# Performance work log

Measured on AMD Instinct MI355X. Metric: run time of the kernel, lower is better.

Reference implementation:

```python
import jax, jax.numpy as jnp
import numpy as np
from jax import lax

B = 16
DEPTH = 24
D_MODEL = 192
D_INNER = 384   # expand=2
D_STATE = 16
D_CONV = 4
DT_RANK = 12    # ceil(192/16)
PATCH = 16
EPS = 1e-5


def setup_inputs() -> dict:
    key = jax.random.key(0)
    ks = jax.random.split(key, 24)
    def n(k, shape, s):
        return jax.random.normal(k, shape, jnp.float32) * s
    inp = {}
    inp["x_img"] = jax.random.normal(ks[0], (B, 3, 256, 256), jnp.float32)
    inp["z_img"] = jax.random.normal(ks[1], (B, 3, 128, 128), jnp.float32)
    # patch embed conv
    inp["patch_w"] = n(ks[2], (D_MODEL, 3, PATCH, PATCH), 0.02)
    inp["patch_b"] = jnp.zeros((D_MODEL,), jnp.float32)
    # abs pos embeds (token counts fixed by module: 256 for x, 64 for z)
    inp["pos_x"] = n(ks[3], (1, 256, D_MODEL), 0.02)
    inp["pos_z"] = n(ks[4], (1, 64, D_MODEL), 0.02)
    # per-layer norms (LayerNorm, rms_norm=False)
    inp["ln_w"] = jnp.ones((DEPTH, D_MODEL), jnp.float32)
    inp["ln_b"] = jnp.zeros((DEPTH, D_MODEL), jnp.float32)
    # Mamba mixer params (stacked over depth)
    inp["in_w"] = n(ks[5], (DEPTH, 2 * D_INNER, D_MODEL), 0.05)          # in_proj (no bias)
    inp["conv_w"] = n(ks[6], (DEPTH, D_INNER, D_CONV), 0.2)              # depthwise conv1d
    inp["conv_b"] = jnp.zeros((DEPTH, D_INNER), jnp.float32)
    inp["xproj_w"] = n(ks[7], (DEPTH, DT_RANK + 2 * D_STATE, D_INNER), 0.05)  # x_proj (no bias)
    inp["dt_w"] = n(ks[8], (DEPTH, D_INNER, DT_RANK), 0.1)               # dt_proj weight
    # dt bias ~ inverse-softplus of dt in [1e-3, 0.1] (Mamba init)
    dt = jnp.exp(jax.random.uniform(ks[9], (DEPTH, D_INNER)) * (np.log(0.1) - np.log(1e-3)) + np.log(1e-3))
    inp["dt_b"] = dt + jnp.log(-jnp.expm1(-dt))
    # A_log init: log(1..d_state) per channel
    inp["A_log"] = jnp.log(jnp.tile(jnp.arange(1, D_STATE + 1, dtype=jnp.float32), (DEPTH, D_INNER, 1)))
    inp["D_skip"] = jnp.ones((DEPTH, D_INNER), jnp.float32)
    inp["out_w"] = n(ks[10], (DEPTH, D_MODEL, D_INNER), 0.05)            # out_proj (no bias)
    inp["fnorm_w"] = jnp.ones((D_MODEL,), jnp.float32)
    inp["fnorm_b"] = jnp.zeros((D_MODEL,), jnp.float32)
    return inp


def _layer_norm(x, w, b):
    mu = jnp.mean(x, axis=-1, keepdims=True)
    var = jnp.mean(jnp.square(x - mu), axis=-1, keepdims=True)
    return (x - mu) * lax.rsqrt(var + EPS) * w + b


def _patch_embed(img, w, b):
    # Conv2d stride=patch, then flatten HW -> tokens
    y = lax.conv_general_dilated(img, w, (PATCH, PATCH), 'VALID',
                                 dimension_numbers=('NCHW', 'OIHW', 'NCHW'))
    y = y + b[None, :, None, None]
    Bn, D, H, W = y.shape
    return y.reshape(Bn, D, H * W).transpose(0, 2, 1)  # (B, HW, D)


def _ssm_scan(dA, dBu):
    # h_t = dA_t * h_{t-1} + dBu_t, parallel over time via associative scan
    def comb(e1, e2):
        a1, b1 = e1
        a2, b2 = e2
        return a2 * a1, a2 * b1 + b2
    _, h = lax.associative_scan(comb, (dA, dBu), axis=1)
    return h  # (B, L, D_INNER, D_STATE)


def _mamba(h, in_w, conv_w, conv_b, xproj_w, dt_w, dt_b, A_log, D_skip, out_w):
    # h: (B, L, D_MODEL)
    xz = h @ in_w.T                                   # (B, L, 2*D_INNER)
    xc, zg = jnp.split(xz, 2, axis=-1)
    # causal depthwise conv over time
    xt = xc.transpose(0, 2, 1)                        # (B, D_INNER, L)
    xt = lax.conv_general_dilated(xt, conv_w[:, None, :], (1,), [(D_CONV - 1, 0)],
                                  feature_group_count=D_INNER,
                                  dimension_numbers=('NCH', 'OIH', 'NCH'))
    xt = xt + conv_b[None, :, None]
    xc = jax.nn.silu(xt).transpose(0, 2, 1)           # (B, L, D_INNER)
    dbl = xc @ xproj_w.T                              # (B, L, dt_rank + 2*d_state)
    dt, Bm, Cm = jnp.split(dbl, [DT_RANK, DT_RANK + D_STATE], axis=-1)
    dt = jax.nn.softplus(dt @ dt_w.T + dt_b)          # (B, L, D_INNER)
    A = -jnp.exp(A_log)                               # (D_INNER, D_STATE)
    dA = jnp.exp(dt[..., None] * A)                   # (B, L, D_INNER, D_STATE)
    dBu = dt[..., None] * Bm[:, :, None, :] * xc[..., None]
    hs = _ssm_scan(dA, dBu)
    y = jnp.einsum('bldn,bln->bld', hs, Cm) + xc * D_skip
    y = y * jax.nn.silu(zg)
    return y @ out_w.T                                # (B, L, D_MODEL)


def reference(x_img, z_img, patch_w, patch_b, pos_x, pos_z, ln_w, ln_b,
              in_w, conv_w, conv_b, xproj_w, dt_w, dt_b, A_log, D_skip,
              out_w, fnorm_w, fnorm_b):
    x_tok = _patch_embed(x_img, patch_w, patch_b) + pos_x   # (B, 256, D)
    z_tok = _patch_embed(z_img, patch_w, patch_b) + pos_z   # (B, 64, D)
    hidden = jnp.concatenate([z_tok, x_tok], axis=1)        # (B, 320, D)
    residual = None
    for i in range(DEPTH):
        # fused add-norm prenorm: residual = hidden + residual; hidden = LN(residual)
        residual = hidden if residual is None else hidden + residual
        h_n = _layer_norm(residual, ln_w[i], ln_b[i])
        hidden = _mamba(h_n, in_w[i], conv_w[i], conv_b[i], xproj_w[i],
                        dt_w[i], dt_b[i], A_log[i], D_skip[i], out_w[i])
    residual = residual + hidden
    return _layer_norm(residual, fnorm_w, fnorm_b)          # (B, 320, D), final_pool_type='none'
```

## Files before the change

### kernel.cpp

```cpp
#include <hip/hip_runtime.h>
#include <hip/hip_bf16.h>

#define BB 16
#define DEPTH 24
#define DM 192
#define DI 384
#define DS 16
#define DC 4
#define DTR 12
#define LL 320
#define NX 256
#define NZ 64
#define NT (BB * LL)
#define NC 10
#define LC 32
#define EPSV 1e-5f

__device__ inline float siluf(float x) { return x / (1.f + __expf(-x)); }
__device__ inline float softplusf(float x) {
    return (x > 20.f) ? x : log1pf(expf(x));
}
__device__ inline float wave_sum64(float v) {
    #pragma unroll
    for (int o = 32; o > 0; o >>= 1) v += __shfl_xor(v, o);
    return v;
}

__global__ __launch_bounds__(256) void ln_gemm(const float* __restrict__ hidden,
                                               const float* __restrict__ resin,
                                               float* __restrict__ resout,
                                               const float* __restrict__ lnw,
                                               const float* __restrict__ lnb,
                                               size_t lnoff,
                                               const float* __restrict__ w,
                                               size_t woff,
                                               float* __restrict__ out,
                                               int first) {
    __shared__ float xs[32][196];
    __shared__ float ws[128][52];
    int t0 = blockIdx.x * 32;
    int j0 = blockIdx.y * 128;
    {
        int tt = threadIdx.x >> 3;
        int l8 = threadIdx.x & 7;
        size_t base = (size_t)(t0 + tt) * DM;
        float v[24];
        float s = 0.f;
        #pragma unroll
        for (int j = 0; j < 24; j++) {
            int e = l8 + 8 * j;
            float x = hidden[base + e];
            if (!first) x += resin[base + e];
            v[j] = x;
            s += x;
        }
        s += __shfl_xor(s, 1); s += __shfl_xor(s, 2); s += __shfl_xor(s, 4);
        float mu = s * (1.f / 192.f);
        float q = 0.f;
        #pragma unroll
        for (int j = 0; j < 24; j++) { float d = v[j] - mu; q += d * d; }
        q += __shfl_xor(q, 1); q += __shfl_xor(q, 2); q += __shfl_xor(q, 4);
        float inv = rsqrtf(q * (1.f / 192.f) + EPSV);
        #pragma unroll
        for (int j = 0; j < 24; j++) {
            int e = l8 + 8 * j;
            if (blockIdx.y == 0) resout[base + e] = v[j];
            xs[tt][e] = (v[j] - mu) * inv * lnw[lnoff + e] + lnb[lnoff + e];
        }
    }
    __syncthreads();
    int lane = threadIdx.x & 63;
    int wv = threadIdx.x >> 6;
    float acc[8][2];
    #pragma unroll
    for (int t = 0; t < 8; t++) { acc[t][0] = 0.f; acc[t][1] = 0.f; }
    for (int kt = 0; kt < 192; kt += 48) {
        for (int idx = threadIdx.x; idx < 128 * 12; idx += 256) {
            int jj = idx / 12, kc = idx % 12;
            float4 v4 = *(const float4*)&w[woff + (size_t)(j0 + jj) * 192 + kt + kc * 4];
            *(float4*)&ws[jj][kc * 4] = v4;
        }
        __syncthreads();
        #pragma unroll 2
        for (int kk = 0; kk < 48; kk += 4) {
            float4 xv[8];
            #pragma unroll
            for (int t = 0; t < 8; t++)
                xv[t] = *(const float4*)&xs[wv * 8 + t][kt + kk];
            #pragma unroll
            for (int o = 0; o < 2; o++) {
                float4 wv4 = *(const float4*)&ws[lane + 64 * o][kk];
                #pragma unroll
                for (int t = 0; t < 8; t++)
                    acc[t][o] += xv[t].x * wv4.x + xv[t].y * wv4.y
                               + xv[t].z * wv4.z + xv[t].w * wv4.w;
            }
        }
        __syncthreads();
    }
    #pragma unroll
    for (int t = 0; t < 8; t++)
        #pragma unroll
        for (int o = 0; o < 2; o++)
            out[(size_t)(t0 + wv * 8 + t) * 768 + j0 + lane + 64 * o] = acc[t][o];
}

template<int K, int KT, int NO>
__global__ __launch_bounds__(256) void gemm_rt(const float* __restrict__ x,
                                               const float* __restrict__ w,
                                               size_t woff,
                                               float* __restrict__ out, int N) {
    constexpr int NCOL = 64 * NO;
    constexpr int KC = KT / 4;
    __shared__ float xs[32][KT + 4];
    __shared__ float ws[NCOL][KT + 4];
    int t0 = blockIdx.x * 32;
    int j0 = blockIdx.y * NCOL;
    int lane = threadIdx.x & 63;
    int wv = threadIdx.x >> 6;
    float acc[8][NO];
    #pragma unroll
    for (int t = 0; t < 8; t++)
        #pragma unroll
        for (int o = 0; o < NO; o++) acc[t][o] = 0.f;

    for (int kt = 0; kt < K; kt += KT) {
        for (int idx = threadIdx.x; idx < 32 * KC; idx += 256) {
            int tt = idx / KC, kc = idx % KC;
            float4 v = *(const float4*)&x[(size_t)(t0 + tt) * K + kt + kc * 4];
            *(float4*)&xs[tt][kc * 4] = v;
        }
        for (int idx = threadIdx.x; idx < NCOL * KC; idx += 256) {
            int jj = idx / KC, kc = idx % KC;
            float4 v = *(const float4*)&w[woff + (size_t)(j0 + jj) * K + kt + kc * 4];
            *(float4*)&ws[jj][kc * 4] = v;
        }
        __syncthreads();
        #pragma unroll 2
        for (int kk = 0; kk < KT; kk += 4) {
            float4 xv[8];
            #pragma unroll
            for (int t = 0; t < 8; t++)
                xv[t] = *(const float4*)&xs[wv * 8 + t][kk];
            #pragma unroll
            for (int o = 0; o < NO; o++) {
                float4 wv4 = *(const float4*)&ws[lane + 64 * o][kk];
                #pragma unroll
                for (int t = 0; t < 8; t++)
                    acc[t][o] += xv[t].x * wv4.x + xv[t].y * wv4.y
                               + xv[t].z * wv4.z + xv[t].w * wv4.w;
            }
        }
        __syncthreads();
    }
    #pragma unroll
    for (int t = 0; t < 8; t++)
        #pragma unroll
        for (int o = 0; o < NO; o++)
            out[(size_t)(t0 + wv * 8 + t) * N + j0 + lane + 64 * o] = acc[t][o];
}

__global__ __launch_bounds__(256) void patch_rt(const float* __restrict__ x_img,
                                                const float* __restrict__ z_img,
                                                const float* __restrict__ w,
                                                const float* __restrict__ bias,
                                                const float* __restrict__ pos_x,
                                                const float* __restrict__ pos_z,
                                                float* __restrict__ hidden) {
    __shared__ float xs[32][100];
    __shared__ float ws[64][100];
    bool isx = blockIdx.x < (BB * NX / 32);
    const float* img = isx ? x_img : z_img;
    const float* pos = isx ? pos_x : pos_z;
    int side = isx ? 16 : 8;
    int tok_off = isx ? NZ : 0;
    int ntok = side * side;
    int pt0 = (isx ? blockIdx.x : blockIdx.x - BB * NX / 32) * 32;
    int j0 = blockIdx.y * 64;
    int S = side * 16;
    int lane = threadIdx.x & 63;
    int wv = threadIdx.x >> 6;
    float acc[8];
    #pragma unroll
    for (int t = 0; t < 8; t++) acc[t] = 0.f;

    for (int kt = 0; kt < 768; kt += 96) {
        for (int idx = threadIdx.x; idx < 32 * 24; idx += 256) {
            int tt = idx / 24, kc = idx % 24;
            int k = kt + kc * 4;
            int c = k >> 8, p = k & 255, pi = p >> 4, pj = p & 15;
            int patch = pt0 + tt;
            int b = patch / ntok, t = patch % ntok;
            int ph = t / side, pw = t % side;
            float4 v = *(const float4*)&img[((size_t)(b * 3 + c) * S + ph * 16 + pi) * S
                                            + pw * 16 + pj];
            *(float4*)&xs[tt][kc * 4] = v;
        }
        for (int idx = threadIdx.x; idx < 64 * 24; idx += 256) {
            int jj = idx / 24, kc = idx % 24;
            float4 v = *(const float4*)&w[(size_t)(j0 + jj) * 768 + kt + kc * 4];
            *(float4*)&ws[jj][kc * 4] = v;
        }
        __syncthreads();
        #pragma unroll 2
        for (int kk = 0; kk < 96; kk += 4) {
            float4 xv[8];
            #pragma unroll
            for (int t = 0; t < 8; t++)
                xv[t] = *(const float4*)&xs[wv * 8 + t][kk];
            float4 wv4 = *(const float4*)&ws[lane][kk];
            #pragma unroll
            for (int t = 0; t < 8; t++)
                acc[t] += xv[t].x * wv4.x + xv[t].y * wv4.y
                        + xv[t].z * wv4.z + xv[t].w * wv4.w;
        }
        __syncthreads();
    }
    float bj = bias[j0 + lane];
    #pragma unroll
    for (int t = 0; t < 8; t++) {
        int patch = pt0 + wv * 8 + t;
        int b = patch / ntok, tk = patch % ntok;
        hidden[((size_t)b * LL + tok_off + tk) * DM + j0 + lane] =
            acc[t] + bj + pos[(size_t)tk * DM + j0 + lane];
    }
}

__global__ __launch_bounds__(256) void xpd_kernel(const float* __restrict__ xz,
                                                  const float* __restrict__ cw,
                                                  const float* __restrict__ cb,
                                                  const float* __restrict__ xpw,
                                                  const float* __restrict__ dtw,
                                                  const float* __restrict__ dtbias,
                                                  float* __restrict__ xc,
                                                  float* __restrict__ dbl,
                                                  float* __restrict__ dtbuf,
                                                  int layer) {
    __shared__ float smem[5760];
    float* xs   = smem;
    float* ws   = smem + 832;
    float* sdbl = smem;
    float* sdtw = smem + 768;

    int t0 = blockIdx.x * 16;
    int l0 = t0 % LL;
    int lane = threadIdx.x & 63;
    int wv = threadIdx.x >> 6;
    const float* cwl = cw  + (size_t)layer * DI * DC;
    const float* cbl = cb  + (size_t)layer * DI;
    const float* xpl = xpw + (size_t)layer * 44 * DI;
    float acc[4] = {0.f, 0.f, 0.f, 0.f};

    for (int kt = 0; kt < DI; kt += 48) {
        for (int idx = threadIdx.x; idx < 16 * 48; idx += 256) {
            int tt = idx / 48, kk = idx % 48;
            int d = kt + kk;
            float a = cbl[d];
            #pragma unroll
            for (int r = 0; r < 4; r++) {
                int l = l0 + tt - 3 + r;
                float v = (l >= 0) ? xz[(size_t)(t0 + tt - 3 + r) * 768 + d] : 0.f;
                a += cwl[d * 4 + r] * v;
            }
            a = siluf(a);
            xs[tt * 52 + kk] = a;
            xc[(size_t)(t0 + tt) * DI + d] = a;
        }
        for (int idx = threadIdx.x; idx < 64 * 12; idx += 256) {
            int jj = idx / 12, kc = idx % 12;
            float4 v = make_float4(0.f, 0.f, 0.f, 0.f);
            if (jj < 44)
                v = *(const float4*)&xpl[(size_t)jj * DI + kt + kc * 4];
            *(float4*)&ws[jj * 52 + kc * 4] = v;
        }
        __syncthreads();
        const float* wr0 = ws + lane * 52;
        #pragma unroll 4
        for (int kk = 0; kk < 48; kk += 4) {
            float4 xv0 = *(const float4*)&xs[(wv * 4 + 0) * 52 + kk];
            float4 xv1 = *(const float4*)&xs[(wv * 4 + 1) * 52 + kk];
            float4 xv2 = *(const float4*)&xs[(wv * 4 + 2) * 52 + kk];
            float4 xv3 = *(const float4*)&xs[(wv * 4 + 3) * 52 + kk];
            float4 wv4 = *(const float4*)&wr0[kk];
            acc[0] += xv0.x * wv4.x + xv0.y * wv4.y + xv0.z * wv4.z + xv0.w * wv4.w;
            acc[1] += xv1.x * wv4.x + xv1.y * wv4.y + xv1.z * wv4.z + xv1.w * wv4.w;
            acc[2] += xv2.x * wv4.x + xv2.y * wv4.y + xv2.z * wv4.z + xv2.w * wv4.w;
            acc[3] += xv3.x * wv4.x + xv3.y * wv4.y + xv3.z * wv4.z + xv3.w * wv4.w;
        }
        __syncthreads();
    }
    if (lane < 44) {
        #pragma unroll
        for (int t = 0; t < 4; t++) {
            sdbl[(wv * 4 + t) * 48 + lane] = acc[t];
            dbl[(size_t)(t0 + wv * 4 + t) * 44 + lane] = acc[t];
        }
    }
    const float* dwl = dtw + (size_t)layer * DI * DTR;
    for (int idx = threadIdx.x; idx < DI * DTR; idx += 256) {
        int d = idx / 12, r = idx % 12;
        sdtw[d * 13 + r] = dwl[idx];
    }
    __syncthreads();
    const float* dbb = dtbias + (size_t)layer * DI;
    for (int idx = threadIdx.x; idx < 16 * DI; idx += 256) {
        int tt = idx / DI, d = idx % DI;
        float a = dbb[d];
        const float* br = sdbl + tt * 48;
        const float* wr = sdtw + d * 13;
        #pragma unroll
        for (int r = 0; r < 12; r++) a += br[r] * wr[r];
        dtbuf[(size_t)(t0 + tt) * DI + d] = softplusf(a);
    }
}

__global__ __launch_bounds__(256) void scanA(const float* __restrict__ dt,
                                             const float* __restrict__ xc,
                                             const float* __restrict__ dbl,
                                             const float* __restrict__ A_log,
                                             float* __restrict__ Pout,
                                             float* __restrict__ Hout,
                                             size_t aoff) {
    int Q = blockIdx.x * 64 + (threadIdx.x >> 2);
    int n0 = threadIdx.x & 3;
    int d = Q % DI;
    int bc = Q / DI;
    int b = bc / NC, c = bc % NC;
    float4 Al = *(const float4*)&A_log[aoff + (size_t)d * DS + n0 * 4];
    float A0 = -expf(Al.x), A1 = -expf(Al.y), A2 = -expf(Al.z), A3 = -expf(Al.w);
    float h0 = 0.f, h1 = 0.f, h2 = 0.f, h3 = 0.f;
    float P0 = 1.f, P1 = 1.f, P2 = 1.f, P3 = 1.f;
    int tbase = b * LL + c * LC;
    for (int l = 0; l < LC; l++) {
        size_t t = (size_t)tbase + l;
        float dtv = dt[t * DI + d];
        float xcv = xc[t * DI + d];
        float4 B4 = *(const float4*)&dbl[t * 44 + DTR + n0 * 4];
        float s = dtv * xcv;
        float e0 = __expf(dtv * A0), e1 = __expf(dtv * A1);
        float e2 = __expf(dtv * A2), e3 = __expf(dtv * A3);
        h0 = e0 * h0 + s * B4.x;  P0 *= e0;
        h1 = e1 * h1 + s * B4.y;  P1 *= e1;
        h2 = e2 * h2 + s * B4.z;  P2 *= e2;
        h3 = e3 * h3 + s * B4.w;  P3 *= e3;
    }
    size_t gi = (size_t)Q * 16 + n0 * 4;
    *(float4*)&Pout[gi] = make_float4(P0, P1, P2, P3);
    *(float4*)&Hout[gi] = make_float4(h0, h1, h2, h3);
}

__global__ __launch_bounds__(256) void scanC(const float* __restrict__ dt,
                                             const float* xc,
                                             const float* __restrict__ dbl,
                                             const float* __restrict__ xz,
                                             const float* __restrict__ A_log,
                                             const float* __restrict__ Dskip,
                                             const float* __restrict__ Pin,
                                             const float* __restrict__ Hin,
                                             float* y,
                                             size_t aoff, size_t doff) {
    int Q = blockIdx.x * 64 + (threadIdx.x >> 2);
    int n0 = threadIdx.x & 3;
    int d = Q % DI;
    int bc = Q / DI;
    int b = bc / NC, c = bc % NC;
    float h0 = 0.f, h1 = 0.f, h2 = 0.f, h3 = 0.f;
    for (int cc = 0; cc < c; cc++) {
        size_t gi = ((size_t)(b * NC + cc) * DI + d) * 16 + n0 * 4;
        float4 P4 = *(const float4*)&Pin[gi];
        float4 H4 = *(const float4*)&Hin[gi];
        h0 = P4.x * h0 + H4.x;
        h1 = P4.y * h1 + H4.y;
        h2 = P4.z * h2 + H4.z;
        h3 = P4.w * h3 + H4.w;
    }
    float4 Al = *(const float4*)&A_log[aoff + (size_t)d * DS + n0 * 4];
    float A0 = -expf(Al.x), A1 = -expf(Al.y), A2 = -expf(Al.z), A3 = -expf(Al.w);
    float Dv = Dskip[doff + d];
    int tbase = b * LL + c * LC;
    for (int l = 0; l < LC; l++) {
        size_t t = (size_t)tbase + l;
        float dtv = dt[t * DI + d];
        float xcv = xc[t * DI + d];
        float4 B4 = *(const float4*)&dbl[t * 44 + DTR + n0 * 4];
        float4 C4 = *(const float4*)&dbl[t * 44 + DTR + DS + n0 * 4];
        float s = dtv * xcv;
        float e0 = __expf(dtv * A0), e1 = __expf(dtv * A1);
        float e2 = __expf(dtv * A2), e3 = __expf(dtv * A3);
        h0 = e0 * h0 + s * B4.x;
        h1 = e1 * h1 + s * B4.y;
        h2 = e2 * h2 + s * B4.z;
        h3 = e3 * h3 + s * B4.w;
        float p = h0 * C4.x + h1 * C4.y + h2 * C4.z + h3 * C4.w;
        p += __shfl_xor(p, 1);
        p += __shfl_xor(p, 2);
        if (n0 == 0) {
            float zg = xz[t * (2 * DI) + DI + d];
            y[t * DI + d] = (p + xcv * Dv) * siluf(zg);
        }
    }
}

__global__ __launch_bounds__(256) void final_kernel(const float* __restrict__ hidden,
                                                    const float* __restrict__ residual,
                                                    const float* __restrict__ w,
                                                    const float* __restrict__ bias,
                                                    float* __restrict__ out) {
    int t = blockIdx.x * 4 + (threadIdx.x >> 6);
    int lane = threadIdx.x & 63;
    size_t base = (size_t)t * DM;
    float a = residual[base + lane]       + hidden[base + lane];
    float b = residual[base + 64 + lane]  + hidden[base + 64 + lane];
    float c = residual[base + 128 + lane] + hidden[base + 128 + lane];
    float mu = wave_sum64(a + b + c) * (1.f / 192.f);
    float va = a - mu, vb = b - mu, vc = c - mu;
    float var = wave_sum64(va * va + vb * vb + vc * vc) * (1.f / 192.f);
    float inv = rsqrtf(var + EPSV);
    out[base + lane]       = va * inv * w[lane]       + bias[lane];
    out[base + 64 + lane]  = vb * inv * w[64 + lane]  + bias[64 + lane];
    out[base + 128 + lane] = vc * inv * w[128 + lane] + bias[128 + lane];
}

extern "C" void kernel_launch(void* const* d_in, const int* in_sizes, int n_in,
                              void* d_out, int out_size, void* d_ws, size_t ws_size,
                              hipStream_t stream) {
    const float* x_img   = (const float*)d_in[0];
    const float* z_img   = (const float*)d_in[1];
    const float* patch_w = (const float*)d_in[2];
    const float* patch_b = (const float*)d_in[3];
    const float* pos_x   = (const float*)d_in[4];
    const float* pos_z   = (const float*)d_in[5];
    const float* ln_w    = (const float*)d_in[6];
    const float* ln_b    = (const float*)d_in[7];
    const float* in_w    = (const float*)d_in[8];
    const float* conv_w  = (const float*)d_in[9];
    const float* conv_b  = (const float*)d_in[10];
    const float* xproj_w = (const float*)d_in[11];
    const float* dt_w    = (const float*)d_in[12];
    const float* dt_b    = (const float*)d_in[13];
    const float* A_log   = (const float*)d_in[14];
    const float* D_skip  = (const float*)d_in[15];
    const float* out_w   = (const float*)d_in[16];
    const float* fnorm_w = (const float*)d_in[17];
    const float* fnorm_b = (const float*)d_in[18];

    float* hidden   = (float*)d_ws;
    float* residual = hidden   + (size_t)NT * DM;
    float* xz       = residual + (size_t)NT * DM;
    float* xc       = xz       + (size_t)NT * 2 * DI;
    float* dbl      = xc       + (size_t)NT * DI;
    float* dtbuf    = dbl      + (size_t)NT * 44;
    float* scanP    = dtbuf    + (size_t)NT * DI;
    float* scanH    = scanP    + (size_t)BB * NC * DI * 16;
    float* yb       = xc;
    float* resalt   = (float*)d_out;

    {
        dim3 gp((BB * NX + BB * NZ) / 32, 3);
        patch_rt<<<gp, 256, 0, stream>>>(x_img, z_img, patch_w, patch_b,
                                         pos_x, pos_z, hidden);
    }

    const int scan_blocks = BB * NC * DI / 64;
    for (int i = 0; i < DEPTH; i++) {
        const float* resin = (i % 2) ? resalt : residual;
        float* resout      = (i % 2) ? residual : resalt;
        {
            dim3 g(NT / 32, 6);
            ln_gemm<<<g, 256, 0, stream>>>(
                hidden, resin, resout, ln_w, ln_b, (size_t)i * DM,
                in_w, (size_t)i * 768 * 192, xz, i == 0 ? 1 : 0);
        }
        xpd_kernel<<<NT / 16, 256, 0, stream>>>(
            xz, conv_w, conv_b, xproj_w, dt_w, dt_b, xc, dbl, dtbuf, i);
        scanA<<<scan_blocks, 256, 0, stream>>>(
            dtbuf, xc, dbl, A_log, scanP, scanH, (size_t)i * DI * DS);
        scanC<<<scan_blocks, 256, 0, stream>>>(
            dtbuf, xc, dbl, xz, A_log, D_skip, scanP, scanH, yb,
            (size_t)i * DI * DS, (size_t)i * DI);
        {
            dim3 g(NT / 32, 3);
            gemm_rt<384, 96, 1><<<g, 256, 0, stream>>>(
                yb, out_w, (size_t)i * 192 * 384, hidden, 192);
        }
    }

    final_kernel<<<NT / 4, 256, 0, stream>>>(hidden, residual, fnorm_w, fnorm_b,
                                             (float*)d_out);
}
```

Measured before the change: 4.285 ms.

## Use 4x4 register micro-tiles in GEMM kernels and halve out-proj/patch block size

Reworks the thread-to-output mapping in the LN+in_proj GEMM, the out_proj GEMM and the patch-embed GEMM so each thread computes a 4x4 tile (4 tokens by 4 columns) instead of 8 tokens by one or two columns. This balances shared-memory loads between x and w fragments and increases FMA per LDS. The out_proj and patch kernels now run with 128 threads per block (2 waves) covering the same 32x64 tile. The trade-off is fewer waves per block to hide latency, and strided global stores (8 lanes per row) instead of fully contiguous 64-wide rows.

```diff
diff --git a/kernel.cpp b/kernel.cpp
--- a/kernel.cpp
+++ b/kernel.cpp
@@ -71,9 +71,13 @@
     __syncthreads();
     int lane = threadIdx.x & 63;
     int wv = threadIdx.x >> 6;
-    float acc[8][2];
-    #pragma unroll
-    for (int t = 0; t < 8; t++) { acc[t][0] = 0.f; acc[t][1] = 0.f; }
+    int r = lane >> 3;
+    int c = lane & 7;
+    float acc[4][4];
+    #pragma unroll
+    for (int i = 0; i < 4; i++)
+        #pragma unroll
+        for (int j = 0; j < 4; j++) acc[i][j] = 0.f;
     for (int kt = 0; kt < 192; kt += 48) {
         for (int idx = threadIdx.x; idx < 128 * 12; idx += 256) {
             int jj = idx / 12, kc = idx % 12;
@@ -83,90 +87,91 @@
         __syncthreads();
         #pragma unroll 2
         for (int kk = 0; kk < 48; kk += 4) {
-            float4 xv[8];
-            #pragma unroll
-            for (int t = 0; t < 8; t++)
-                xv[t] = *(const float4*)&xs[wv * 8 + t][kt + kk];
-            #pragma unroll
-            for (int o = 0; o < 2; o++) {
-                float4 wv4 = *(const float4*)&ws[lane + 64 * o][kk];
+            float4 xv[4];
+            #pragma unroll
+            for (int i = 0; i < 4; i++)
+                xv[i] = *(const float4*)&xs[r + 8 * i][kt + kk];
+            #pragma unroll
+            for (int j = 0; j < 4; j++) {
+                float4 w4 = *(const float4*)&ws[wv * 32 + c + 8 * j][kk];
                 #pragma unroll
-                for (int t = 0; t < 8; t++)
-                    acc[t][o] += xv[t].x * wv4.x + xv[t].y * wv4.y
-                               + xv[t].z * wv4.z + xv[t].w * wv4.w;
+                for (int i = 0; i < 4; i++)
+                    acc[i][j] += xv[i].x * w4.x + xv[i].y * w4.y
+                               + xv[i].z * w4.z + xv[i].w * w4.w;
             }
         }
         __syncthreads();
     }
     #pragma unroll
-    for (int t = 0; t < 8; t++)
-        #pragma unroll
-        for (int o = 0; o < 2; o++)
-            out[(size_t)(t0 + wv * 8 + t) * 768 + j0 + lane + 64 * o] = acc[t][o];
-}
-
-template<int K, int KT, int NO>
-__global__ __launch_bounds__(256) void gemm_rt(const float* __restrict__ x,
-                                               const float* __restrict__ w,
-                                               size_t woff,
-                                               float* __restrict__ out, int N) {
-    constexpr int NCOL = 64 * NO;
+    for (int i = 0; i < 4; i++)
+        #pragma unroll
+        for (int j = 0; j < 4; j++)
+            out[(size_t)(t0 + r + 8 * i) * 768 + j0 + wv * 32 + c + 8 * j] = acc[i][j];
+}
+
+template<int K, int KT>
+__global__ __launch_bounds__(128) void gemm_rt2(const float* __restrict__ x,
+                                                const float* __restrict__ w,
+                                                size_t woff,
+                                                float* __restrict__ out, int N) {
     constexpr int KC = KT / 4;
     __shared__ float xs[32][KT + 4];
-    __shared__ float ws[NCOL][KT + 4];
+    __shared__ float ws[64][KT + 4];
     int t0 = blockIdx.x * 32;
-    int j0 = blockIdx.y * NCOL;
+    int j0 = blockIdx.y * 64;
     int lane = threadIdx.x & 63;
     int wv = threadIdx.x >> 6;
-    float acc[8][NO];
-    #pragma unroll
-    for (int t = 0; t < 8; t++)
-        #pragma unroll
-        for (int o = 0; o < NO; o++) acc[t][o] = 0.f;
+    int r = lane >> 3;
+    int c = lane & 7;
+    float acc[4][4];
+    #pragma unroll
+    for (int i = 0; i < 4; i++)
+        #pragma unroll
+        for (int j = 0; j < 4; j++) acc[i][j] = 0.f;
 
     for (int kt = 0; kt < K; kt += KT) {
-        for (int idx = threadIdx.x; idx < 32 * KC; idx += 256) {
+        for (int idx = threadIdx.x; idx < 32 * KC; idx += 128) {
             int tt = idx / KC, kc = idx % KC;
-            float4 v = *(const float4*)&x[(size_t)(t0 + tt) * K + kt + kc * 4];
-            *(float4*)&xs[tt][kc * 4] = v;
-        }
-        for (int idx = threadIdx.x; idx < NCOL * KC; idx += 256) {
+            *(float4*)&xs[tt][kc * 4] =
+                *(const float4*)&x[(size_t)(t0 + tt) * K + kt + kc * 4];
+        }
+        for (int idx = threadIdx.x; idx < 64 * KC; idx += 128) {
             int jj = idx / KC, kc = idx % KC;
-            float4 v = *(const float4*)&w[woff + (size_t)(j0 + jj) * K + kt + kc * 4];
-            *(float4*)&ws[jj][kc * 4] = v;
+            *(float4*)&ws[jj][kc * 4] =
+                *(const float4*)&w[woff + (size_t)(j0 + jj) * K + kt + kc * 4];
         }
         __syncthreads();
         #pragma unroll 2
         for (int kk = 0; kk < KT; kk += 4) {
-            float4 xv[8];
-            #pragma unroll
-            for (int t = 0; t < 8; t++)
-                xv[t] = *(const float4*)&xs[wv * 8 + t][kk];
-            #pragma unroll
-            for (int o = 0; o < NO; o++) {
-                float4 wv4 = *(const float4*)&ws[lane + 64 * o][kk];
+            float4 xv[4];
+            #pragma unroll
+            for (int i = 0; i < 4; i++)
+                xv[i] = *(const float4*)&xs[r + 8 * i][kk];
+            #pragma unroll
+            for (int j = 0; j < 4; j++) {
+                float4 w4 = *(const float4*)&ws[wv * 32 + c + 8 * j][kk];
                 #pragma unroll
-                for (int t = 0; t < 8; t++)
-                    acc[t][o] += xv[t].x * wv4.x + xv[t].y * wv4.y
-                               + xv[t].z * wv4.z + xv[t].w * wv4.w;
+                for (int i = 0; i < 4; i++)
+                    acc[i][j] += xv[i].x * w4.x + xv[i].y * w4.y
+                               + xv[i].z * w4.z + xv[i].w * w4.w;
             }
         }
         __syncthreads();
     }
     #pragma unroll
-    for (int t = 0; t < 8; t++)
-        #pragma unroll
-        for (int o = 0; o < NO; o++)
-            out[(size_t)(t0 + wv * 8 + t) * N + j0 + lane + 64 * o] = acc[t][o];
-}
-
-__global__ __launch_bounds__(256) void patch_rt(const float* __restrict__ x_img,
-                                                const float* __restrict__ z_img,
-                                                const float* __restrict__ w,
-                                                const float* __restrict__ bias,
-                                                const float* __restrict__ pos_x,
-                                                const float* __restrict__ pos_z,
-                                                float* __restrict__ hidden) {
+    for (int i = 0; i < 4; i++)
+        #pragma unroll
+        for (int j = 0; j < 4; j++)
+            out[(size_t)(t0 + r + 8 * i) * N + j0 + wv * 32 + c + 8 * j] = acc[i][j];
+}
+
+__global__ __launch_bounds__(128) void patch_rt2(const float* __restrict__ x_img,
+                                                 const float* __restrict__ z_img,
+                                                 const float* __restrict__ w,
+                                                 const float* __restrict__ bias,
+                                                 const float* __restrict__ pos_x,
+                                                 const float* __restrict__ pos_z,
+                                                 float* __restrict__ hidden) {
     __shared__ float xs[32][100];
     __shared__ float ws[64][100];
     bool isx = blockIdx.x < (BB * NX / 32);
@@ -180,49 +185,59 @@
     int S = side * 16;
     int lane = threadIdx.x & 63;
     int wv = threadIdx.x >> 6;
-    float acc[8];
-    #pragma unroll
-    for (int t = 0; t < 8; t++) acc[t] = 0.f;
+    int r = lane >> 3;
+    int c = lane & 7;
+    float acc[4][4];
+    #pragma unroll
+    for (int i = 0; i < 4; i++)
+        #pragma unroll
+        for (int j = 0; j < 4; j++) acc[i][j] = 0.f;
 
     for (int kt = 0; kt < 768; kt += 96) {
-        for (int idx = threadIdx.x; idx < 32 * 24; idx += 256) {
+        for (int idx = threadIdx.x; idx < 32 * 24; idx += 128) {
             int tt = idx / 24, kc = idx % 24;
             int k = kt + kc * 4;
-            int c = k >> 8, p = k & 255, pi = p >> 4, pj = p & 15;
+            int ci = k >> 8, p = k & 255, pi = p >> 4, pj = p & 15;
             int patch = pt0 + tt;
             int b = patch / ntok, t = patch % ntok;
             int ph = t / side, pw = t % side;
-            float4 v = *(const float4*)&img[((size_t)(b * 3 + c) * S + ph * 16 + pi) * S
-                                            + pw * 16 + pj];
-            *(float4*)&xs[tt][kc * 4] = v;
-        }
-        for (int idx = threadIdx.x; idx < 64 * 24; idx += 256) {
+            *(float4*)&xs[tt][kc * 4] =
+                *(const float4*)&img[((size_t)(b * 3 + ci) * S + ph * 16 + pi) * S
+                                     + pw * 16 + pj];
+        }
+        for (int idx = threadIdx.x; idx < 64 * 24; idx += 128) {
             int jj = idx / 24, kc = idx % 24;
-            float4 v = *(const float4*)&w[(size_t)(j0 + jj) * 768 + kt + kc * 4];
-            *(float4*)&ws[jj][kc * 4] = v;
+            *(float4*)&ws[jj][kc * 4] =
+                *(const float4*)&w[(size_t)(j0 + jj) * 768 + kt + kc * 4];
         }
         __syncthreads();
         #pragma unroll 2
         for (int kk = 0; kk < 96; kk += 4) {
-            float4 xv[8];
-            #pragma unroll
-            for (int t = 0; t < 8; t++)
-                xv[t] = *(const float4*)&xs[wv * 8 + t][kk];
-            float4 wv4 = *(const float4*)&ws[lane][kk];
-            #pragma unroll
-            for (int t = 0; t < 8; t++)
-                acc[t] += xv[t].x * wv4.x + xv[t].y * wv4.y
-                        + xv[t].z * wv4.z + xv[t].w * wv4.w;
-        }
-        __syncthreads();
-    }
-    float bj = bias[j0 + lane];
-    #pragma unroll
-    for (int t = 0; t < 8; t++) {
-        int patch = pt0 + wv * 8 + t;
+            float4 xv[4];
+            #pragma unroll
+            for (int i = 0; i < 4; i++)
+                xv[i] = *(const float4*)&xs[r + 8 * i][kk];
+            #pragma unroll
+            for (int j = 0; j < 4; j++) {
+                float4 w4 = *(const float4*)&ws[wv * 32 + c + 8 * j][kk];
+                #pragma unroll
+                for (int i = 0; i < 4; i++)
+                    acc[i][j] += xv[i].x * w4.x + xv[i].y * w4.y
+                               + xv[i].z * w4.z + xv[i].w * w4.w;
+            }
+        }
+        __syncthreads();
+    }
+    #pragma unroll
+    for (int i = 0; i < 4; i++) {
+        int patch = pt0 + r + 8 * i;
         int b = patch / ntok, tk = patch % ntok;
-        hidden[((size_t)b * LL + tok_off + tk) * DM + j0 + lane] =
-            acc[t] + bj + pos[(size_t)tk * DM + j0 + lane];
+        #pragma unroll
+        for (int j = 0; j < 4; j++) {
+            int col = j0 + wv * 32 + c + 8 * j;
+            hidden[((size_t)b * LL + tok_off + tk) * DM + col] =
+                acc[i][j] + bias[col] + pos[(size_t)tk * DM + col];
+        }
     }
 }
 
@@ -257,10 +272,10 @@
             int d = kt + kk;
             float a = cbl[d];
             #pragma unroll
-            for (int r = 0; r < 4; r++) {
-                int l = l0 + tt - 3 + r;
-                float v = (l >= 0) ? xz[(size_t)(t0 + tt - 3 + r) * 768 + d] : 0.f;
-                a += cwl[d * 4 + r] * v;
+            for (int rr = 0; rr < 4; rr++) {
+                int l = l0 + tt - 3 + rr;
+                float v = (l >= 0) ? xz[(size_t)(t0 + tt - 3 + rr) * 768 + d] : 0.f;
+                a += cwl[d * 4 + rr] * v;
             }
             a = siluf(a);
             xs[tt * 52 + kk] = a;
@@ -298,8 +313,8 @@
     }
     const float* dwl = dtw + (size_t)layer * DI * DTR;
     for (int idx = threadIdx.x; idx < DI * DTR; idx += 256) {
-        int d = idx / 12, r = idx % 12;
-        sdtw[d * 13 + r] = dwl[idx];
+        int d = idx / 12, rr = idx % 12;
+        sdtw[d * 13 + rr] = dwl[idx];
     }
     __syncthreads();
     const float* dbb = dtbias + (size_t)layer * DI;
@@ -309,7 +324,7 @@
         const float* br = sdbl + tt * 48;
         const float* wr = sdtw + d * 13;
         #pragma unroll
-        for (int r = 0; r < 12; r++) a += br[r] * wr[r];
+        for (int rr = 0; rr < 12; rr++) a += br[rr] * wr[rr];
         dtbuf[(size_t)(t0 + tt) * DI + d] = softplusf(a);
     }
 }
@@ -457,8 +472,8 @@
 
     {
         dim3 gp((BB * NX + BB * NZ) / 32, 3);
-        patch_rt<<<gp, 256, 0, stream>>>(x_img, z_img, patch_w, patch_b,
-                                         pos_x, pos_z, hidden);
+        patch_rt2<<<gp, 128, 0, stream>>>(x_img, z_img, patch_w, patch_b,
+                                          pos_x, pos_z, hidden);
     }
 
     const int scan_blocks = BB * NC * DI / 64;
@@ -480,7 +495,7 @@
             (size_t)i * DI * DS, (size_t)i * DI);
         {
             dim3 g(NT / 32, 3);
-            gemm_rt<384, 96, 1><<<g, 256, 0, stream>>>(
+            gemm_rt2<384, 96><<<g, 128, 0, stream>>>(
                 yb, out_w, (size_t)i * 192 * 384, hidden, 192);
         }
     }
```

Result: slower. 4.545 ms (+6.1%).
